# Kernel optimization log

Hardware: AMD Instinct MI355X
Metric: run time of the kernel (lower is better)

The kernel has to match this reference:

```python
import jax, jax.numpy as jnp
import numpy as np

N_NODES = 100000
N_EDGES = 1200000
N_GRAPHS = 512
F_IN = 7
H = 64
N_CLASSES = 10


def _xavier(key, shape):
    fan_in, fan_out = shape[0], shape[1]
    limit = float(np.sqrt(6.0 / (fan_in + fan_out)))
    return jax.random.uniform(key, shape, jnp.float32, -limit, limit)


def setup_inputs() -> dict:
    key = jax.random.key(0)
    ks = jax.random.split(key, 16)
    x = jax.random.normal(ks[0], (N_NODES, F_IN), jnp.float32)
    edge_index = jax.random.randint(ks[1], (2, N_EDGES), 0, N_NODES, jnp.int64)
    batch = jnp.sort(jax.random.randint(ks[2], (N_NODES,), 0, N_GRAPHS, jnp.int64))
    d = {
        'x': x, 'edge_index': edge_index, 'batch': batch,
        'W_emb': _xavier(ks[3], (F_IN, H)), 'b_emb': jnp.zeros((H,), jnp.float32),
        'eps1': jnp.zeros((), jnp.float32),
        'W1a': _xavier(ks[4], (H, 2 * H)), 'b1a': jnp.zeros((2 * H,), jnp.float32),
        'W1b': _xavier(ks[5], (2 * H, H)), 'b1b': jnp.zeros((H,), jnp.float32),
        'eps2': jnp.zeros((), jnp.float32),
        'W2a': _xavier(ks[6], (H, 2 * H)), 'b2a': jnp.zeros((2 * H,), jnp.float32),
        'W2b': _xavier(ks[7], (2 * H, H)), 'b2b': jnp.zeros((H,), jnp.float32),
        'eps3': jnp.zeros((), jnp.float32),
        'W3a': _xavier(ks[8], (H, 2 * H)), 'b3a': jnp.zeros((2 * H,), jnp.float32),
        'W3b': _xavier(ks[9], (2 * H, H)), 'b3b': jnp.zeros((H,), jnp.float32),
        'Wc1': _xavier(ks[10], (2 * H, H)), 'bc1': jnp.zeros((H,), jnp.float32),
        'Wc2': _xavier(ks[11], (H, N_CLASSES)), 'bc2': jnp.zeros((N_CLASSES,), jnp.float32),
    }
    return d


def _gin_layer(x, eps, Wa, ba, Wb, bb, src, dst):
    # scatter-add aggregation of source features into destination nodes
    agg = jax.ops.segment_sum(x[src], dst, num_segments=N_NODES)
    h = (1.0 + eps) * x + agg
    h = jax.nn.relu(h @ Wa + ba) @ Wb + bb
    return jax.nn.elu(h)  # dropout is identity in eval mode


def reference(x, edge_index, batch,
              W_emb, b_emb,
              eps1, W1a, b1a, W1b, b1b,
              eps2, W2a, b2a, W2b, b2b,
              eps3, W3a, b3a, W3b, b3b,
              Wc1, bc1, Wc2, bc2):
    src, dst = edge_index[0], edge_index[1]
    h = x @ W_emb + b_emb                      # [N, H]
    h = _gin_layer(h, eps1, W1a, b1a, W1b, b1b, src, dst)
    h = _gin_layer(h, eps2, W2a, b2a, W2b, b2b, src, dst)
    h = _gin_layer(h, eps3, W3a, b3a, W3b, b3b, src, dst)
    # global mean + max pool per graph
    sums = jax.ops.segment_sum(h, batch, num_segments=N_GRAPHS)
    cnts = jax.ops.segment_sum(jnp.ones((h.shape[0], 1), h.dtype), batch, num_segments=N_GRAPHS)
    mean = sums / jnp.maximum(cnts, 1.0)
    mx = jax.ops.segment_max(h, batch, num_segments=N_GRAPHS)
    g = jnp.concatenate([mean, mx], axis=1)    # [G, 2H]
    out = jax.nn.relu(g @ Wc1 + bc1) @ Wc2 + bc2
    return out
```

## Files before the change

kernel.cpp:

```cpp
#include <hip/hip_runtime.h>
#include <hip/hip_bf16.h>
#include <math.h>

#define N_NODES 100000
#define N_EDGES 1200000
#define N_GRAPHS 512
#define NBUCKET 98
#define TILE 2048
#define CSR_CAP 16384

typedef __bf16 bf16x8 __attribute__((ext_vector_type(8)));
typedef float f32x4 __attribute__((ext_vector_type(4)));

__device__ __forceinline__ unsigned f2ord(float f) {
  unsigned u = __float_as_uint(f);
  return (u & 0x80000000u) ? ~u : (u | 0x80000000u);
}
__device__ __forceinline__ float ord2f(unsigned u) {
  return (u & 0x80000000u) ? __uint_as_float(u & 0x7fffffffu) : __uint_as_float(~u);
}

__global__ void bucket_hist_kernel(const int* __restrict__ dst, int* __restrict__ bcnt) {
  __shared__ int c[128];
  int t = threadIdx.x;
  if (t < 128) c[t] = 0;
  __syncthreads();
  for (int e = blockIdx.x * 256 + t; e < N_EDGES; e += gridDim.x * 256)
    atomicAdd(&c[dst[e] >> 10], 1);
  __syncthreads();
  if (t < NBUCKET && c[t] > 0) atomicAdd(&bcnt[t], c[t]);
}

__global__ void bucket_scan_kernel(const int* __restrict__ bcnt,
                                   int* __restrict__ bbase,
                                   int* __restrict__ bcursor,
                                   int* __restrict__ rowp) {
  __shared__ int s[128];
  int t = threadIdx.x;
  int own = (t < NBUCKET) ? bcnt[t] : 0;
  s[t] = own;
  __syncthreads();
  for (int o = 1; o < 128; o <<= 1) {
    int v = (t >= o) ? s[t - o] : 0;
    __syncthreads();
    s[t] += v;
    __syncthreads();
  }
  if (t < NBUCKET) {
    int excl = s[t] - own;
    bbase[t] = excl;
    bcursor[t] = excl;
  }
  if (t == 0) {
    bbase[NBUCKET] = N_EDGES;
    rowp[N_NODES] = N_EDGES;
  }
}

__global__ void partition_kernel(const int* __restrict__ src, const int* __restrict__ dst,
                                 int* __restrict__ bcursor, unsigned* __restrict__ ent) {
  __shared__ int cnt[128];
  __shared__ int cnt2[128];
  __shared__ int lstart[128];
  __shared__ int gbase[128];
  __shared__ int s[128];
  __shared__ unsigned sorted[TILE];
  __shared__ unsigned char bid[TILE];
  int t = threadIdx.x;
  int e0 = blockIdx.x * TILE;
  if (t < 128) { cnt[t] = 0; cnt2[t] = 0; }
  __syncthreads();

  unsigned v[8];
  int b[8];
#pragma unroll
  for (int u = 0; u < 8; ++u) {
    int e = e0 + u * 256 + t;
    b[u] = -1;
    if (e < N_EDGES) {
      int d = dst[e];
      b[u] = d >> 10;
      v[u] = (unsigned)src[e] | ((unsigned)(d & 1023) << 17);
      atomicAdd(&cnt[b[u]], 1);
    }
  }
  __syncthreads();
  if (t < 128) s[t] = cnt[t];
  __syncthreads();
  for (int o = 1; o < 128; o <<= 1) {
    int x = (t >= o && t < 128) ? s[t - o] : 0;
    __syncthreads();
    if (t < 128) s[t] += x;
    __syncthreads();
  }
  if (t < 128) lstart[t] = s[t] - cnt[t];
  __syncthreads();
  if (t < NBUCKET) gbase[t] = (cnt[t] > 0) ? atomicAdd(&bcursor[t], cnt[t]) : 0;
  __syncthreads();
#pragma unroll
  for (int u = 0; u < 8; ++u) {
    if (b[u] >= 0) {
      int p = lstart[b[u]] + atomicAdd(&cnt2[b[u]], 1);
      sorted[p] = v[u];
      bid[p] = (unsigned char)b[u];
    }
  }
  __syncthreads();
  int ntile = min(TILE, N_EDGES - e0);
  for (int i = t; i < ntile; i += 256) {
    int bb = bid[i];
    ent[gbase[bb] + (i - lstart[bb])] = sorted[i];
  }
}

__launch_bounds__(256)
__global__ void bucket_csr_kernel(const unsigned* __restrict__ ent,
                                  const int* __restrict__ bbase,
                                  int* __restrict__ rowp,
                                  int* __restrict__ ssrc) {
  __shared__ unsigned le[CSR_CAP];
  __shared__ int deg[1024];
  __shared__ int excl[1024];
  __shared__ int ws[256];
  int t = threadIdx.x;
  int b = blockIdx.x;
  int base = bbase[b];
  int cntb = bbase[b + 1] - base;
#pragma unroll
  for (int k = 0; k < 4; ++k) deg[t * 4 + k] = 0;
  __syncthreads();
  for (int i = t; i < cntb; i += 256) {
    unsigned e = ent[base + i];
    if (i < CSR_CAP) le[i] = e;
    atomicAdd(&deg[e >> 17], 1);
  }
  __syncthreads();
  int d0 = deg[t * 4], d1 = deg[t * 4 + 1], d2 = deg[t * 4 + 2], d3 = deg[t * 4 + 3];
  int sum4 = d0 + d1 + d2 + d3;
  ws[t] = sum4;
  __syncthreads();
  for (int o = 1; o < 256; o <<= 1) {
    int x = (t >= o) ? ws[t - o] : 0;
    __syncthreads();
    ws[t] += x;
    __syncthreads();
  }
  int run = ws[t] - sum4;
  excl[t * 4] = run; run += d0;
  excl[t * 4 + 1] = run; run += d1;
  excl[t * 4 + 2] = run; run += d2;
  excl[t * 4 + 3] = run;
  __syncthreads();
  int node0 = b << 10;
#pragma unroll
  for (int k = 0; k < 4; ++k) {
    int i = t * 4 + k;
    int n = node0 + i;
    if (n < N_NODES) rowp[n] = base + excl[i];
    deg[i] = excl[i];
  }
  __syncthreads();
  for (int i = t; i < cntb; i += 256) {
    unsigned e = (i < CSR_CAP) ? le[i] : ent[base + i];
    int p = atomicAdd(&deg[e >> 17], 1);
    ssrc[base + p] = (int)(e & 0x1FFFFu);
  }
}

__global__ void embed_kernel(const float* __restrict__ x,
                             const float* __restrict__ W,
                             const float* __restrict__ b,
                             __bf16* __restrict__ h) {
  __shared__ float Ws[7 * 64];
  __shared__ float bs[64];
  int t = threadIdx.x;
  for (int i = t; i < 7 * 64; i += 256) Ws[i] = W[i];
  if (t < 64) bs[t] = b[t];
  __syncthreads();
  int gid = blockIdx.x * 256 + t;
  int n = gid >> 6, f = gid & 63;
  const float* xr = x + n * 7;
  float acc = bs[f];
#pragma unroll
  for (int k = 0; k < 7; ++k) acc = fmaf(xr[k], Ws[k * 64 + f], acc);
  h[gid] = (__bf16)acc;
}

__global__ void convert_all_kernel(const float* __restrict__ W1a, const float* __restrict__ W1b,
                                   const float* __restrict__ W2a, const float* __restrict__ W2b,
                                   const float* __restrict__ W3a, const float* __restrict__ W3b,
                                   __bf16* __restrict__ wp,
                                   float* gsum, unsigned* gmax, int* gcnt) {
  int o = blockIdx.x * 256 + threadIdx.x;
  if (o < N_GRAPHS * 64) {
    gsum[o] = 0.0f;
    gmax[o] = 0x407FFFFFu;
  }
  if (o < N_GRAPHS) gcnt[o] = 0;
  int L = o >> 14, q = o & 16383;
  const float* Wa = (L == 0) ? W1a : (L == 1) ? W2a : W3a;
  const float* Wb = (L == 0) ? W1b : (L == 1) ? W2b : W3b;
  if (q < 8192) {
    int j = q & 7, c = (q >> 3) & 15, kc = (q >> 7) & 3, kt = (q >> 9) & 1, nt = q >> 10;
    wp[o] = (__bf16)Wa[(kt * 32 + kc * 8 + j) * 128 + nt * 16 + c];
  } else {
    int p = q - 8192;
    int j = p & 7, c = (p >> 3) & 15, kc = (p >> 7) & 3, kt = (p >> 9) & 3, nt2 = p >> 11;
    wp[o] = (__bf16)Wb[(kt * 32 + kc * 8 + j) * 64 + nt2 * 16 + c];
  }
}

__launch_bounds__(256)
__global__ void gin_fused3_kernel(const __bf16* __restrict__ hin,
                                  __bf16* __restrict__ hout,
                                  const int* __restrict__ row_ptr,
                                  const int* __restrict__ ssrc,
                                  const float* __restrict__ eps_p,
                                  const __bf16* __restrict__ W1p,
                                  const float* __restrict__ b1,
                                  const __bf16* __restrict__ W2p,
                                  const float* __restrict__ b2) {
  __shared__ __bf16 As[64 * 72];
  __shared__ __bf16 Hs[64 * 136];
  int t = threadIdx.x, lane = t & 63, wv = t >> 6;
  int c = lane & 15, kc = lane >> 4;
  int m0 = wv * 16;
  float epsv = 1.0f + eps_p[0];
  int n0b = blockIdx.x * 64;
  int n0w = n0b + m0;

  int rp = row_ptr[min(n0w + min(lane, 16), N_NODES)];

  for (int rr = 0; rr < 8; ++rr) {
    int rA = rr, rB = rr + 8;
    int nA = n0w + rA, nB = n0w + rB;
    int jA = __builtin_amdgcn_readfirstlane(__shfl(rp, rA));
    int eA = __builtin_amdgcn_readfirstlane(__shfl(rp, rA + 1));
    int jB = __builtin_amdgcn_readfirstlane(__shfl(rp, rB));
    int eB = __builtin_amdgcn_readfirstlane(__shfl(rp, rB + 1));
    float accA = (nA < N_NODES) ? epsv * (float)hin[(size_t)nA * 64 + lane] : 0.0f;
    float accB = (nB < N_NODES) ? epsv * (float)hin[(size_t)nB * 64 + lane] : 0.0f;
    while (jA + 4 <= eA && jB + 4 <= eB) {
      int a0 = ssrc[jA], a1 = ssrc[jA + 1], a2 = ssrc[jA + 2], a3 = ssrc[jA + 3];
      int b0 = ssrc[jB], b1_ = ssrc[jB + 1], b2_ = ssrc[jB + 2], b3_ = ssrc[jB + 3];
      float fa0 = (float)hin[(size_t)a0 * 64 + lane];
      float fa1 = (float)hin[(size_t)a1 * 64 + lane];
      float fa2 = (float)hin[(size_t)a2 * 64 + lane];
      float fa3 = (float)hin[(size_t)a3 * 64 + lane];
      float fb0 = (float)hin[(size_t)b0 * 64 + lane];
      float fb1 = (float)hin[(size_t)b1_ * 64 + lane];
      float fb2 = (float)hin[(size_t)b2_ * 64 + lane];
      float fb3 = (float)hin[(size_t)b3_ * 64 + lane];
      accA += (fa0 + fa1) + (fa2 + fa3);
      accB += (fb0 + fb1) + (fb2 + fb3);
      jA += 4; jB += 4;
    }
    for (; jA + 4 <= eA; jA += 4) {
      int a0 = ssrc[jA], a1 = ssrc[jA + 1], a2 = ssrc[jA + 2], a3 = ssrc[jA + 3];
      float f0 = (float)hin[(size_t)a0 * 64 + lane];
      float f1 = (float)hin[(size_t)a1 * 64 + lane];
      float f2 = (float)hin[(size_t)a2 * 64 + lane];
      float f3 = (float)hin[(size_t)a3 * 64 + lane];
      accA += (f0 + f1) + (f2 + f3);
    }
    for (; jB + 4 <= eB; jB += 4) {
      int b0 = ssrc[jB], b1v = ssrc[jB + 1], b2v = ssrc[jB + 2], b3v = ssrc[jB + 3];
      float f0 = (float)hin[(size_t)b0 * 64 + lane];
      float f1 = (float)hin[(size_t)b1v * 64 + lane];
      float f2 = (float)hin[(size_t)b2v * 64 + lane];
      float f3 = (float)hin[(size_t)b3v * 64 + lane];
      accB += (f0 + f1) + (f2 + f3);
    }
    for (; jA < eA; ++jA) accA += (float)hin[(size_t)ssrc[jA] * 64 + lane];
    for (; jB < eB; ++jB) accB += (float)hin[(size_t)ssrc[jB] * 64 + lane];
    As[(m0 + rA) * 72 + lane] = (__bf16)accA;
    As[(m0 + rB) * 72 + lane] = (__bf16)accB;
  }

  bf16x8 a1_0 = *(const bf16x8*)&As[(m0 + c) * 72 + 0 * 32 + kc * 8];
  bf16x8 a1_1 = *(const bf16x8*)&As[(m0 + c) * 72 + 1 * 32 + kc * 8];
  f32x4 acc1[8];
#pragma unroll
  for (int nt = 0; nt < 8; ++nt) {
    float bv = b1[nt * 16 + c];
    f32x4 acc = {bv, bv, bv, bv};
    bf16x8 bf0 = *(const bf16x8*)&W1p[(nt * 2 + 0) * 512 + kc * 128 + c * 8];
    bf16x8 bf1 = *(const bf16x8*)&W1p[(nt * 2 + 1) * 512 + kc * 128 + c * 8];
    acc = __builtin_amdgcn_mfma_f32_16x16x32_bf16(a1_0, bf0, acc, 0, 0, 0);
    acc = __builtin_amdgcn_mfma_f32_16x16x32_bf16(a1_1, bf1, acc, 0, 0, 0);
    acc1[nt] = acc;
  }
#pragma unroll
  for (int nt = 0; nt < 8; ++nt) {
#pragma unroll
    for (int r = 0; r < 4; ++r) {
      Hs[(m0 + kc * 4 + r) * 136 + nt * 16 + c] = (__bf16)fmaxf(acc1[nt][r], 0.0f);
    }
  }

  bf16x8 a2[4];
#pragma unroll
  for (int kt = 0; kt < 4; ++kt)
    a2[kt] = *(const bf16x8*)&Hs[(m0 + c) * 136 + kt * 32 + kc * 8];
#pragma unroll
  for (int nt2 = 0; nt2 < 4; ++nt2) {
    float bv = b2[nt2 * 16 + c];
    f32x4 acc = {bv, bv, bv, bv};
#pragma unroll
    for (int kt = 0; kt < 4; ++kt) {
      bf16x8 bf = *(const bf16x8*)&W2p[(nt2 * 4 + kt) * 512 + kc * 128 + c * 8];
      acc = __builtin_amdgcn_mfma_f32_16x16x32_bf16(a2[kt], bf, acc, 0, 0, 0);
    }
#pragma unroll
    for (int r = 0; r < 4; ++r) {
      int g = n0b + m0 + kc * 4 + r;
      if (g < N_NODES) {
        float o = acc[r];
        hout[(size_t)g * 64 + nt2 * 16 + c] = (__bf16)((o > 0.0f) ? o : expm1f(o));
      }
    }
  }
}

__global__ void pool_kernel(const __bf16* __restrict__ h,
                            const int* __restrict__ batch,
                            float* gsum, unsigned* gmax, int* gcnt) {
  int lane = threadIdx.x & 63;
  int wave = (blockIdx.x * blockDim.x + threadIdx.x) >> 6;
  int nwaves = (gridDim.x * blockDim.x) >> 6;
  int chunk = (N_NODES + nwaves - 1) / nwaves;
  int n0 = wave * chunk;
  int n1 = min(n0 + chunk, N_NODES);
  if (n0 >= N_NODES) return;
  int cur = batch[n0];
  float s = 0.0f, m = -2.0f;
  int cnt = 0;
  for (int n = n0; n < n1; ++n) {
    int g = batch[n];
    if (g != cur) {
      atomicAdd(&gsum[cur * 64 + lane], s);
      atomicMax(&gmax[cur * 64 + lane], f2ord(m));
      if (lane == 0) atomicAdd(&gcnt[cur], cnt);
      cur = g; s = 0.0f; m = -2.0f; cnt = 0;
    }
    float v = (float)h[(size_t)n * 64 + lane];
    s += v;
    m = fmaxf(m, v);
    ++cnt;
  }
  atomicAdd(&gsum[cur * 64 + lane], s);
  atomicMax(&gmax[cur * 64 + lane], f2ord(m));
  if (lane == 0) atomicAdd(&gcnt[cur], cnt);
}

__global__ void cls_kernel(const float* __restrict__ gsum,
                           const unsigned* __restrict__ gmax,
                           const int* __restrict__ gcnt,
                           const float* __restrict__ Wc1,
                           const float* __restrict__ bc1,
                           const float* __restrict__ Wc2,
                           const float* __restrict__ bc2,
                           float* __restrict__ out) {
  __shared__ float gv[128];
  __shared__ float tv[64];
  int g = blockIdx.x, l = threadIdx.x;
  float cnt = fmaxf((float)gcnt[g], 1.0f);
  gv[l] = gsum[g * 64 + l] / cnt;
  gv[64 + l] = ord2f(gmax[g * 64 + l]);
  __syncthreads();
  float acc = bc1[l];
#pragma unroll 8
  for (int k = 0; k < 128; ++k) acc = fmaf(gv[k], Wc1[k * 64 + l], acc);
  tv[l] = fmaxf(acc, 0.0f);
  __syncthreads();
  if (l < 10) {
    float o = bc2[l];
#pragma unroll
    for (int k = 0; k < 64; ++k) o = fmaf(tv[k], Wc2[k * 10 + l], o);
    out[g * 10 + l] = o;
  }
}

extern "C" void kernel_launch(void* const* d_in, const int* in_sizes, int n_in,
                              void* d_out, int out_size, void* d_ws, size_t ws_size,
                              hipStream_t stream) {
  const float* x     = (const float*)d_in[0];
  const int*   ei    = (const int*)d_in[1];
  const int*   batch = (const int*)d_in[2];
  const float* W_emb = (const float*)d_in[3];
  const float* b_emb = (const float*)d_in[4];
  const float* eps1  = (const float*)d_in[5];
  const float* W1a   = (const float*)d_in[6];
  const float* b1a   = (const float*)d_in[7];
  const float* W1b   = (const float*)d_in[8];
  const float* b1b   = (const float*)d_in[9];
  const float* eps2  = (const float*)d_in[10];
  const float* W2a   = (const float*)d_in[11];
  const float* b2a   = (const float*)d_in[12];
  const float* W2b   = (const float*)d_in[13];
  const float* b2b   = (const float*)d_in[14];
  const float* eps3  = (const float*)d_in[15];
  const float* W3a   = (const float*)d_in[16];
  const float* b3a   = (const float*)d_in[17];
  const float* W3b   = (const float*)d_in[18];
  const float* b3b   = (const float*)d_in[19];
  const float* Wc1   = (const float*)d_in[20];
  const float* bc1   = (const float*)d_in[21];
  const float* Wc2   = (const float*)d_in[22];
  const float* bc2   = (const float*)d_in[23];
  float* out = (float*)d_out;

  char* w = (char*)d_ws;
  __bf16*   h0   = (__bf16*)w;                     w += (size_t)N_NODES * 64 * 2;
  __bf16*   h1   = (__bf16*)w;                     w += (size_t)N_NODES * 64 * 2;
  float*    gsum = (float*)w;                      w += N_GRAPHS * 64 * 4;
  unsigned* gmax = (unsigned*)w;                   w += N_GRAPHS * 64 * 4;
  int*      gcnt = (int*)w;                        w += N_GRAPHS * 4;
  __bf16*   wp   = (__bf16*)w;                     w += 3 * 16384 * 2;
  int*      bcnt = (int*)w;                        w += 128 * 4;
  int*      bbase= (int*)w;                        w += 136 * 4;
  int*      bcur = (int*)w;                        w += 128 * 4;
  int*      rowp = (int*)w;                        w += (size_t)(N_NODES + 1) * 4;
  unsigned* ent  = (unsigned*)w;                   w += (size_t)N_EDGES * 4;
  int*      ssrc = (int*)w;                        w += (size_t)N_EDGES * 4;

  const int* src = ei;
  const int* dst = ei + N_EDGES;

  const float* epss[3] = {eps1, eps2, eps3};
  const float* bas[3]  = {b1a, b2a, b3a};
  const float* bbs[3]  = {b1b, b2b, b3b};

  hipMemsetAsync(bcnt, 0, 128 * sizeof(int), stream);
  bucket_hist_kernel<<<256, 256, 0, stream>>>(dst, bcnt);
  bucket_scan_kernel<<<1, 128, 0, stream>>>(bcnt, bbase, bcur, rowp);
  partition_kernel<<<(N_EDGES + TILE - 1) / TILE, 256, 0, stream>>>(src, dst, bcur, ent);
  bucket_csr_kernel<<<NBUCKET, 256, 0, stream>>>(ent, bbase, rowp, ssrc);

  convert_all_kernel<<<192, 256, 0, stream>>>(W1a, W1b, W2a, W2b, W3a, W3b, wp,
                                              gsum, gmax, gcnt);
  embed_kernel<<<(N_NODES * 64) / 256, 256, 0, stream>>>(x, W_emb, b_emb, h0);

  __bf16* hbuf[4] = {h0, h1, h0, h1};
  for (int L = 0; L < 3; ++L) {
    gin_fused3_kernel<<<(N_NODES + 63) / 64, 256, 0, stream>>>(
        hbuf[L], hbuf[L + 1], rowp, ssrc, epss[L],
        wp + (size_t)L * 16384, bas[L],
        wp + (size_t)L * 16384 + 8192, bbs[L]);
  }

  pool_kernel<<<512, 256, 0, stream>>>(h1, batch, gsum, gmax, gcnt);
  cls_kernel<<<N_GRAPHS, 64, 0, stream>>>(gsum, gmax, gcnt, Wc1, bc1, Wc2, bc2, out);
}
```

Before: 423.6 us.

## Gather two bf16 features per lane over split half-waves; use finer CSR buckets

The CSR build now uses 512-node buckets (196 blocks instead of 98), which doubles parallelism in the bucket CSR kernel and halves its shared memory. In the GIN layer, each lane now loads a packed pair of bf16 features with one 32-bit load, and the two half-waves handle alternating neighbours. Their partial sums are combined with a cross-half shuffle. This halves the number of gather load instructions and makes the per-edge loop more parallel. Shared memory is also repacked into a per-wave region reused for both staging buffers. The cost is extra tail-handling branches and the reduction shuffles.

```diff
diff --git a/kernel.cpp b/kernel.cpp
--- a/kernel.cpp
+++ b/kernel.cpp
@@ -5,9 +5,10 @@
 #define N_NODES 100000
 #define N_EDGES 1200000
 #define N_GRAPHS 512
-#define NBUCKET 98
+#define NBUCKET 196
+#define BSHIFT 9
 #define TILE 2048
-#define CSR_CAP 16384
+#define CSR_CAP 8192
 
 typedef __bf16 bf16x8 __attribute__((ext_vector_type(8)));
 typedef float f32x4 __attribute__((ext_vector_type(4)));
@@ -19,14 +20,16 @@
 __device__ __forceinline__ float ord2f(unsigned u) {
   return (u & 0x80000000u) ? __uint_as_float(u & 0x7fffffffu) : __uint_as_float(~u);
 }
+__device__ __forceinline__ float bflo(unsigned u) { return __uint_as_float(u << 16); }
+__device__ __forceinline__ float bfhi(unsigned u) { return __uint_as_float(u & 0xFFFF0000u); }
 
 __global__ void bucket_hist_kernel(const int* __restrict__ dst, int* __restrict__ bcnt) {
-  __shared__ int c[128];
+  __shared__ int c[256];
   int t = threadIdx.x;
-  if (t < 128) c[t] = 0;
+  c[t] = 0;
   __syncthreads();
   for (int e = blockIdx.x * 256 + t; e < N_EDGES; e += gridDim.x * 256)
-    atomicAdd(&c[dst[e] >> 10], 1);
+    atomicAdd(&c[dst[e] >> BSHIFT], 1);
   __syncthreads();
   if (t < NBUCKET && c[t] > 0) atomicAdd(&bcnt[t], c[t]);
 }
@@ -35,12 +38,12 @@
                                    int* __restrict__ bbase,
                                    int* __restrict__ bcursor,
                                    int* __restrict__ rowp) {
-  __shared__ int s[128];
+  __shared__ int s[256];
   int t = threadIdx.x;
   int own = (t < NBUCKET) ? bcnt[t] : 0;
   s[t] = own;
   __syncthreads();
-  for (int o = 1; o < 128; o <<= 1) {
+  for (int o = 1; o < 256; o <<= 1) {
     int v = (t >= o) ? s[t - o] : 0;
     __syncthreads();
     s[t] += v;
@@ -59,16 +62,16 @@
 
 __global__ void partition_kernel(const int* __restrict__ src, const int* __restrict__ dst,
                                  int* __restrict__ bcursor, unsigned* __restrict__ ent) {
-  __shared__ int cnt[128];
-  __shared__ int cnt2[128];
-  __shared__ int lstart[128];
-  __shared__ int gbase[128];
-  __shared__ int s[128];
+  __shared__ int cnt[256];
+  __shared__ int cnt2[256];
+  __shared__ int lstart[256];
+  __shared__ int gbase[256];
+  __shared__ int s[256];
   __shared__ unsigned sorted[TILE];
   __shared__ unsigned char bid[TILE];
   int t = threadIdx.x;
   int e0 = blockIdx.x * TILE;
-  if (t < 128) { cnt[t] = 0; cnt2[t] = 0; }
+  cnt[t] = 0; cnt2[t] = 0;
   __syncthreads();
 
   unsigned v[8];
@@ -79,21 +82,21 @@
     b[u] = -1;
     if (e < N_EDGES) {
       int d = dst[e];
-      b[u] = d >> 10;
-      v[u] = (unsigned)src[e] | ((unsigned)(d & 1023) << 17);
+      b[u] = d >> BSHIFT;
+      v[u] = (unsigned)src[e] | ((unsigned)(d & 511) << 17);
       atomicAdd(&cnt[b[u]], 1);
     }
   }
   __syncthreads();
-  if (t < 128) s[t] = cnt[t];
-  __syncthreads();
-  for (int o = 1; o < 128; o <<= 1) {
-    int x = (t >= o && t < 128) ? s[t - o] : 0;
+  s[t] = cnt[t];
+  __syncthreads();
+  for (int o = 1; o < 256; o <<= 1) {
+    int x = (t >= o) ? s[t - o] : 0;
     __syncthreads();
-    if (t < 128) s[t] += x;
+    s[t] += x;
     __syncthreads();
   }
-  if (t < 128) lstart[t] = s[t] - cnt[t];
+  lstart[t] = s[t] - cnt[t];
   __syncthreads();
   if (t < NBUCKET) gbase[t] = (cnt[t] > 0) ? atomicAdd(&bcursor[t], cnt[t]) : 0;
   __syncthreads();
@@ -119,15 +122,14 @@
                                   int* __restrict__ rowp,
                                   int* __restrict__ ssrc) {
   __shared__ unsigned le[CSR_CAP];
-  __shared__ int deg[1024];
-  __shared__ int excl[1024];
+  __shared__ int deg[512];
+  __shared__ int excl[512];
   __shared__ int ws[256];
   int t = threadIdx.x;
   int b = blockIdx.x;
   int base = bbase[b];
   int cntb = bbase[b + 1] - base;
-#pragma unroll
-  for (int k = 0; k < 4; ++k) deg[t * 4 + k] = 0;
+  deg[t] = 0; deg[t + 256] = 0;
   __syncthreads();
   for (int i = t; i < cntb; i += 256) {
     unsigned e = ent[base + i];
@@ -135,9 +137,9 @@
     atomicAdd(&deg[e >> 17], 1);
   }
   __syncthreads();
-  int d0 = deg[t * 4], d1 = deg[t * 4 + 1], d2 = deg[t * 4 + 2], d3 = deg[t * 4 + 3];
-  int sum4 = d0 + d1 + d2 + d3;
-  ws[t] = sum4;
+  int d0 = deg[t * 2], d1 = deg[t * 2 + 1];
+  int sum2 = d0 + d1;
+  ws[t] = sum2;
   __syncthreads();
   for (int o = 1; o < 256; o <<= 1) {
     int x = (t >= o) ? ws[t - o] : 0;
@@ -145,16 +147,14 @@
     ws[t] += x;
     __syncthreads();
   }
-  int run = ws[t] - sum4;
-  excl[t * 4] = run; run += d0;
-  excl[t * 4 + 1] = run; run += d1;
-  excl[t * 4 + 2] = run; run += d2;
-  excl[t * 4 + 3] = run;
-  __syncthreads();
-  int node0 = b << 10;
-#pragma unroll
-  for (int k = 0; k < 4; ++k) {
-    int i = t * 4 + k;
+  int run = ws[t] - sum2;
+  excl[t * 2] = run; run += d0;
+  excl[t * 2 + 1] = run;
+  __syncthreads();
+  int node0 = b << BSHIFT;
+#pragma unroll
+  for (int k = 0; k < 2; ++k) {
+    int i = t * 2 + k;
     int n = node0 + i;
     if (n < N_NODES) rowp[n] = base + excl[i];
     deg[i] = excl[i];
@@ -211,7 +211,7 @@
 }
 
 __launch_bounds__(256)
-__global__ void gin_fused3_kernel(const __bf16* __restrict__ hin,
+__global__ void gin_fused4_kernel(const __bf16* __restrict__ hin,
                                   __bf16* __restrict__ hout,
                                   const int* __restrict__ row_ptr,
                                   const int* __restrict__ ssrc,
@@ -220,16 +220,20 @@
                                   const float* __restrict__ b1,
                                   const __bf16* __restrict__ W2p,
                                   const float* __restrict__ b2) {
-  __shared__ __bf16 As[64 * 72];
-  __shared__ __bf16 Hs[64 * 136];
+  __shared__ __bf16 SM[4 * 2176];
   int t = threadIdx.x, lane = t & 63, wv = t >> 6;
   int c = lane & 15, kc = lane >> 4;
-  int m0 = wv * 16;
+  int hl2 = (lane & 31) * 2;
+  int par = lane >> 5;
+  __bf16* AsW = &SM[wv * 2176];
+  __bf16* HsW = AsW;
   float epsv = 1.0f + eps_p[0];
   int n0b = blockIdx.x * 64;
-  int n0w = n0b + m0;
+  int n0w = n0b + wv * 16;
 
   int rp = row_ptr[min(n0w + min(lane, 16), N_NODES)];
+
+#define LD2(sidx) (*(const unsigned*)&hin[(size_t)(sidx) * 64 + hl2])
 
   for (int rr = 0; rr < 8; ++rr) {
     int rA = rr, rB = rr + 8;
@@ -238,47 +242,92 @@
     int eA = __builtin_amdgcn_readfirstlane(__shfl(rp, rA + 1));
     int jB = __builtin_amdgcn_readfirstlane(__shfl(rp, rB));
     int eB = __builtin_amdgcn_readfirstlane(__shfl(rp, rB + 1));
-    float accA = (nA < N_NODES) ? epsv * (float)hin[(size_t)nA * 64 + lane] : 0.0f;
-    float accB = (nB < N_NODES) ? epsv * (float)hin[(size_t)nB * 64 + lane] : 0.0f;
-    while (jA + 4 <= eA && jB + 4 <= eB) {
-      int a0 = ssrc[jA], a1 = ssrc[jA + 1], a2 = ssrc[jA + 2], a3 = ssrc[jA + 3];
-      int b0 = ssrc[jB], b1_ = ssrc[jB + 1], b2_ = ssrc[jB + 2], b3_ = ssrc[jB + 3];
-      float fa0 = (float)hin[(size_t)a0 * 64 + lane];
-      float fa1 = (float)hin[(size_t)a1 * 64 + lane];
-      float fa2 = (float)hin[(size_t)a2 * 64 + lane];
-      float fa3 = (float)hin[(size_t)a3 * 64 + lane];
-      float fb0 = (float)hin[(size_t)b0 * 64 + lane];
-      float fb1 = (float)hin[(size_t)b1_ * 64 + lane];
-      float fb2 = (float)hin[(size_t)b2_ * 64 + lane];
-      float fb3 = (float)hin[(size_t)b3_ * 64 + lane];
-      accA += (fa0 + fa1) + (fa2 + fa3);
-      accB += (fb0 + fb1) + (fb2 + fb3);
-      jA += 4; jB += 4;
-    }
-    for (; jA + 4 <= eA; jA += 4) {
-      int a0 = ssrc[jA], a1 = ssrc[jA + 1], a2 = ssrc[jA + 2], a3 = ssrc[jA + 3];
-      float f0 = (float)hin[(size_t)a0 * 64 + lane];
-      float f1 = (float)hin[(size_t)a1 * 64 + lane];
-      float f2 = (float)hin[(size_t)a2 * 64 + lane];
-      float f3 = (float)hin[(size_t)a3 * 64 + lane];
-      accA += (f0 + f1) + (f2 + f3);
-    }
-    for (; jB + 4 <= eB; jB += 4) {
-      int b0 = ssrc[jB], b1v = ssrc[jB + 1], b2v = ssrc[jB + 2], b3v = ssrc[jB + 3];
-      float f0 = (float)hin[(size_t)b0 * 64 + lane];
-      float f1 = (float)hin[(size_t)b1v * 64 + lane];
-      float f2 = (float)hin[(size_t)b2v * 64 + lane];
-      float f3 = (float)hin[(size_t)b3v * 64 + lane];
-      accB += (f0 + f1) + (f2 + f3);
-    }
-    for (; jA < eA; ++jA) accA += (float)hin[(size_t)ssrc[jA] * 64 + lane];
-    for (; jB < eB; ++jB) accB += (float)hin[(size_t)ssrc[jB] * 64 + lane];
-    As[(m0 + rA) * 72 + lane] = (__bf16)accA;
-    As[(m0 + rB) * 72 + lane] = (__bf16)accB;
-  }
-
-  bf16x8 a1_0 = *(const bf16x8*)&As[(m0 + c) * 72 + 0 * 32 + kc * 8];
-  bf16x8 a1_1 = *(const bf16x8*)&As[(m0 + c) * 72 + 1 * 32 + kc * 8];
+    float axA = 0.f, ayA = 0.f, axB = 0.f, ayB = 0.f;
+    if (par == 0) {
+      if (nA < N_NODES) { unsigned u = LD2(nA); axA = epsv * bflo(u); ayA = epsv * bfhi(u); }
+      if (nB < N_NODES) { unsigned u = LD2(nB); axB = epsv * bflo(u); ayB = epsv * bfhi(u); }
+    }
+    while (jA + 8 <= eA && jB + 8 <= eB) {
+      int a0 = ssrc[jA], a1 = ssrc[jA+1], a2 = ssrc[jA+2], a3 = ssrc[jA+3];
+      int a4 = ssrc[jA+4], a5 = ssrc[jA+5], a6 = ssrc[jA+6], a7 = ssrc[jA+7];
+      int b0 = ssrc[jB], b1_ = ssrc[jB+1], b2_ = ssrc[jB+2], b3_ = ssrc[jB+3];
+      int b4 = ssrc[jB+4], b5 = ssrc[jB+5], b6 = ssrc[jB+6], b7 = ssrc[jB+7];
+      unsigned uA0 = LD2(par ? a1 : a0), uA1 = LD2(par ? a3 : a2);
+      unsigned uA2 = LD2(par ? a5 : a4), uA3 = LD2(par ? a7 : a6);
+      unsigned uB0 = LD2(par ? b1_ : b0), uB1 = LD2(par ? b3_ : b2_);
+      unsigned uB2 = LD2(par ? b5 : b4), uB3 = LD2(par ? b7 : b6);
+      axA += (bflo(uA0) + bflo(uA1)) + (bflo(uA2) + bflo(uA3));
+      ayA += (bfhi(uA0) + bfhi(uA1)) + (bfhi(uA2) + bfhi(uA3));
+      axB += (bflo(uB0) + bflo(uB1)) + (bflo(uB2) + bflo(uB3));
+      ayB += (bfhi(uB0) + bfhi(uB1)) + (bfhi(uB2) + bfhi(uB3));
+      jA += 8; jB += 8;
+    }
+    while (jA + 8 <= eA) {
+      int a0 = ssrc[jA], a1 = ssrc[jA+1], a2 = ssrc[jA+2], a3 = ssrc[jA+3];
+      int a4 = ssrc[jA+4], a5 = ssrc[jA+5], a6 = ssrc[jA+6], a7 = ssrc[jA+7];
+      unsigned u0 = LD2(par ? a1 : a0), u1 = LD2(par ? a3 : a2);
+      unsigned u2 = LD2(par ? a5 : a4), u3 = LD2(par ? a7 : a6);
+      axA += (bflo(u0) + bflo(u1)) + (bflo(u2) + bflo(u3));
+      ayA += (bfhi(u0) + bfhi(u1)) + (bfhi(u2) + bfhi(u3));
+      jA += 8;
+    }
+    if (jA + 4 <= eA) {
+      int a0 = ssrc[jA], a1 = ssrc[jA+1], a2 = ssrc[jA+2], a3 = ssrc[jA+3];
+      unsigned u0 = LD2(par ? a1 : a0), u1 = LD2(par ? a3 : a2);
+      axA += bflo(u0) + bflo(u1);
+      ayA += bfhi(u0) + bfhi(u1);
+      jA += 4;
+    }
+    if (jA + 2 <= eA) {
+      int a0 = ssrc[jA], a1 = ssrc[jA+1];
+      unsigned u0 = LD2(par ? a1 : a0);
+      axA += bflo(u0); ayA += bfhi(u0);
+      jA += 2;
+    }
+    if (jA < eA && par == 0) {
+      unsigned u0 = LD2(ssrc[jA]);
+      axA += bflo(u0); ayA += bfhi(u0);
+    }
+    while (jB + 8 <= eB) {
+      int b0 = ssrc[jB], b1_ = ssrc[jB+1], b2_ = ssrc[jB+2], b3_ = ssrc[jB+3];
+      int b4 = ssrc[jB+4], b5 = ssrc[jB+5], b6 = ssrc[jB+6], b7 = ssrc[jB+7];
+      unsigned u0 = LD2(par ? b1_ : b0), u1 = LD2(par ? b3_ : b2_);
+      unsigned u2 = LD2(par ? b5 : b4), u3 = LD2(par ? b7 : b6);
+      axB += (bflo(u0) + bflo(u1)) + (bflo(u2) + bflo(u3));
+      ayB += (bfhi(u0) + bfhi(u1)) + (bfhi(u2) + bfhi(u3));
+      jB += 8;
+    }
+    if (jB + 4 <= eB) {
+      int b0 = ssrc[jB], b1_ = ssrc[jB+1], b2_ = ssrc[jB+2], b3_ = ssrc[jB+3];
+      unsigned u0 = LD2(par ? b1_ : b0), u1 = LD2(par ? b3_ : b2_);
+      axB += bflo(u0) + bflo(u1);
+      ayB += bfhi(u0) + bfhi(u1);
+      jB += 4;
+    }
+    if (jB + 2 <= eB) {
+      int b0 = ssrc[jB], b1_ = ssrc[jB+1];
+      unsigned u0 = LD2(par ? b1_ : b0);
+      axB += bflo(u0); ayB += bfhi(u0);
+      jB += 2;
+    }
+    if (jB < eB && par == 0) {
+      unsigned u0 = LD2(ssrc[jB]);
+      axB += bflo(u0); ayB += bfhi(u0);
+    }
+    axA += __shfl_xor(axA, 32); ayA += __shfl_xor(ayA, 32);
+    axB += __shfl_xor(axB, 32); ayB += __shfl_xor(ayB, 32);
+    if (par == 0) {
+      union { __bf16 b[2]; unsigned u; } pA, pB;
+      pA.b[0] = (__bf16)axA; pA.b[1] = (__bf16)ayA;
+      pB.b[0] = (__bf16)axB; pB.b[1] = (__bf16)ayB;
+      *(unsigned*)&AsW[rA * 72 + hl2] = pA.u;
+      *(unsigned*)&AsW[rB * 72 + hl2] = pB.u;
+    }
+  }
+#undef LD2
+
+  bf16x8 a1_0 = *(const bf16x8*)&AsW[c * 72 + 0 * 32 + kc * 8];
+  bf16x8 a1_1 = *(const bf16x8*)&AsW[c * 72 + 1 * 32 + kc * 8];
   f32x4 acc1[8];
 #pragma unroll
   for (int nt = 0; nt < 8; ++nt) {
@@ -294,14 +343,14 @@
   for (int nt = 0; nt < 8; ++nt) {
 #pragma unroll
     for (int r = 0; r < 4; ++r) {
-      Hs[(m0 + kc * 4 + r) * 136 + nt * 16 + c] = (__bf16)fmaxf(acc1[nt][r], 0.0f);
+      HsW[(kc * 4 + r) * 136 + nt * 16 + c] = (__bf16)fmaxf(acc1[nt][r], 0.0f);
     }
   }
 
   bf16x8 a2[4];
 #pragma unroll
   for (int kt = 0; kt < 4; ++kt)
-    a2[kt] = *(const bf16x8*)&Hs[(m0 + c) * 136 + kt * 32 + kc * 8];
+    a2[kt] = *(const bf16x8*)&HsW[c * 136 + kt * 32 + kc * 8];
 #pragma unroll
   for (int nt2 = 0; nt2 < 4; ++nt2) {
     float bv = b2[nt2 * 16 + c];
@@ -313,7 +362,7 @@
     }
 #pragma unroll
     for (int r = 0; r < 4; ++r) {
-      int g = n0b + m0 + kc * 4 + r;
+      int g = n0b + wv * 16 + kc * 4 + r;
       if (g < N_NODES) {
         float o = acc[r];
         hout[(size_t)g * 64 + nt2 * 16 + c] = (__bf16)((o > 0.0f) ? o : expm1f(o));
@@ -417,9 +466,9 @@
   unsigned* gmax = (unsigned*)w;                   w += N_GRAPHS * 64 * 4;
   int*      gcnt = (int*)w;                        w += N_GRAPHS * 4;
   __bf16*   wp   = (__bf16*)w;                     w += 3 * 16384 * 2;
-  int*      bcnt = (int*)w;                        w += 128 * 4;
-  int*      bbase= (int*)w;                        w += 136 * 4;
-  int*      bcur = (int*)w;                        w += 128 * 4;
+  int*      bcnt = (int*)w;                        w += 256 * 4;
+  int*      bbase= (int*)w;                        w += 260 * 4;
+  int*      bcur = (int*)w;                        w += 256 * 4;
   int*      rowp = (int*)w;                        w += (size_t)(N_NODES + 1) * 4;
   unsigned* ent  = (unsigned*)w;                   w += (size_t)N_EDGES * 4;
   int*      ssrc = (int*)w;                        w += (size_t)N_EDGES * 4;
@@ -431,9 +480,9 @@
   const float* bas[3]  = {b1a, b2a, b3a};
   const float* bbs[3]  = {b1b, b2b, b3b};
 
-  hipMemsetAsync(bcnt, 0, 128 * sizeof(int), stream);
+  hipMemsetAsync(bcnt, 0, 256 * sizeof(int), stream);
   bucket_hist_kernel<<<256, 256, 0, stream>>>(dst, bcnt);
-  bucket_scan_kernel<<<1, 128, 0, stream>>>(bcnt, bbase, bcur, rowp);
+  bucket_scan_kernel<<<1, 256, 0, stream>>>(bcnt, bbase, bcur, rowp);
   partition_kernel<<<(N_EDGES + TILE - 1) / TILE, 256, 0, stream>>>(src, dst, bcur, ent);
   bucket_csr_kernel<<<NBUCKET, 256, 0, stream>>>(ent, bbase, rowp, ssrc);
 
@@ -443,7 +492,7 @@
 
   __bf16* hbuf[4] = {h0, h1, h0, h1};
   for (int L = 0; L < 3; ++L) {
-    gin_fused3_kernel<<<(N_NODES + 63) / 64, 256, 0, stream>>>(
+    gin_fused4_kernel<<<(N_NODES + 63) / 64, 256, 0, stream>>>(
         hbuf[L], hbuf[L + 1], rowp, ssrc, epss[L],
         wp + (size_t)L * 16384, bas[L],
         wp + (size_t)L * 16384 + 8192, bbs[L]);
```

New measurement: 448.7 us. +5.9%, slower.
